# Kernel tuning notes

Measured on AMD Instinct MI355X. Metric: run time of the kernel, lower is better.

Reference implementation:

```python
import jax, jax.numpy as jnp
import numpy as np

CROP_H, CROP_W = 14, 14
MAX_BS = 64  # max boxes per image per level (MoldBatch padding)
NUM_LEVELS = 4


def _crop_and_resize(fmap, boxes, box_indices, ch, cw):
    """Bilinear tf.image.crop_and_resize equivalent.
    fmap: [B,H,W,C]; boxes: [N,4] normalized (y1,x1,y2,x2); box_indices: [N] int32.
    Returns [N,ch,cw,C]; samples outside the image get extrapolation value 0."""
    B, H, W, C = fmap.shape
    y1, x1, y2, x2 = boxes[:, 0], boxes[:, 1], boxes[:, 2], boxes[:, 3]
    ty = jnp.arange(ch, dtype=boxes.dtype) / (ch - 1)
    tx = jnp.arange(cw, dtype=boxes.dtype) / (cw - 1)
    ys = y1[:, None] * (H - 1) + ty[None, :] * ((y2 - y1)[:, None] * (H - 1))  # [N,ch]
    xs = x1[:, None] * (W - 1) + tx[None, :] * ((x2 - x1)[:, None] * (W - 1))  # [N,cw]
    y0f = jnp.floor(ys); x0f = jnp.floor(xs)
    wy = (ys - y0f)[:, :, None, None]  # [N,ch,1,1]
    wx = (xs - x0f)[:, None, :, None]  # [N,1,cw,1]
    y0 = jnp.clip(y0f.astype(jnp.int32), 0, H - 1); y1i = jnp.clip(y0 + 1, 0, H - 1)
    x0 = jnp.clip(x0f.astype(jnp.int32), 0, W - 1); x1i = jnp.clip(x0 + 1, 0, W - 1)
    bi = box_indices[:, None, None]
    g = lambda yi, xi: fmap[bi, yi[:, :, None], xi[:, None, :], :]  # [N,ch,cw,C]
    top = g(y0, x0) * (1 - wx) + g(y0, x1i) * wx
    bot = g(y1i, x0) * (1 - wx) + g(y1i, x1i) * wx
    out = top * (1 - wy) + bot * wy
    valid = ((ys >= 0) & (ys <= H - 1))[:, :, None] & ((xs >= 0) & (xs <= W - 1))[:, None, :]
    return out * valid[..., None].astype(out.dtype)


def setup_inputs() -> dict:
    key = jax.random.key(0)
    ks = jax.random.split(key, 8)
    B, N, C = 4, 128, 256
    sizes = [256, 128, 64, 32]
    inp = {}
    for i, s in enumerate(sizes):
        inp[f"fmap{i}"] = jax.random.normal(ks[i], (B, s, s, C), dtype=jnp.float32)
    ids = jax.random.randint(ks[4], (B, N), 0, NUM_LEVELS).astype(jnp.float32)
    cxy = jax.random.uniform(ks[5], (B, N, 2), minval=0.0, maxval=1024.0)
    wh = jax.random.uniform(ks[6], (B, N, 2), minval=16.0, maxval=256.0)
    cls_id = jnp.zeros((B, N, 1), jnp.float32)
    conf = jnp.full((B, N, 1), 0.9, jnp.float32)
    inp["dist_boxes"] = jnp.concatenate([ids[..., None], cxy, wh, cls_id, conf], axis=-1)
    inp["images"] = jnp.zeros((B, 1024, 1024, 3), jnp.float32)
    return inp


def _forward(fmaps, dist_boxes, images):
    B, N, _ = dist_boxes.shape
    Hi, Wi = images.shape[1], images.shape[2]
    cx, cy, w, h = (dist_boxes[..., 1], dist_boxes[..., 2], dist_boxes[..., 3], dist_boxes[..., 4])
    # NormalizeBoxes: (cx,cy,w,h) pixels -> normalized (y1,x1,y2,x2) for crop_and_resize
    norm_boxes = jnp.stack([
        (cy - h / 2) / (Hi - 1), (cx - w / 2) / (Wi - 1),
        (cy + h / 2) / (Hi - 1), (cx + w / 2) / (Wi - 1)], axis=-1)  # [B,N,4]
    ids = dist_boxes[..., 0]
    flat_boxes = norm_boxes.reshape(B * N, 4)
    box_idx = jnp.repeat(jnp.arange(B, dtype=jnp.int32), N)
    b_idx = jnp.broadcast_to(jnp.arange(B)[:, None], (B, N))
    boxes6 = dist_boxes[..., 1:]  # [B,N,6]
    roi_fmaps, roi_boxes = [], []
    for lvl, fmap in enumerate(fmaps):
        C = fmap.shape[-1]
        mask = ids == lvl  # [B,N] level routing (tf.where/gather_nd equivalent)
        crops = _crop_and_resize(fmap, flat_boxes, box_idx, CROP_H, CROP_W)
        crops = crops.reshape(B, N, CROP_H, CROP_W, C)
        # MoldBatch: scatter level-l boxes densely per image, zero-padded to MAX_BS
        rank = jnp.cumsum(mask.astype(jnp.int32), axis=1) - 1
        dest = jnp.where(mask & (rank < MAX_BS), rank, MAX_BS)  # overflow -> dump slot
        pf = jnp.zeros((B, MAX_BS + 1, CROP_H, CROP_W, C), crops.dtype)
        pf = pf.at[b_idx, dest].set(crops * mask[..., None, None, None].astype(crops.dtype))
        roi_fmaps.append(pf[:, :MAX_BS])
        pb = jnp.zeros((B, MAX_BS + 1, 6), dist_boxes.dtype)
        pb = pb.at[b_idx, dest].set(boxes6 * mask[..., None].astype(boxes6.dtype))
        roi_boxes.append(pb[:, :MAX_BS])
    return jnp.stack(roi_fmaps), jnp.concatenate(roi_boxes, axis=1)


def reference(fmap0, fmap1, fmap2, fmap3, dist_boxes, images):
    return _forward([fmap0, fmap1, fmap2, fmap3], dist_boxes, images)
```

## Files before the change

### kernel.cpp

```cpp
#include <hip/hip_runtime.h>

#define CROP 14
#define MAXBS 64
#define NLVL 4
#define BDIM 4
#define NBOX 128
#define CCH 256

__global__ void roi_meta_kernel(const float* __restrict__ db,
                                int* __restrict__ slot_map,
                                float* __restrict__ out1) {
    int b = blockIdx.x;
    int t = threadIdx.x;
    __shared__ int lvl_arr[NBOX];
    __shared__ int smap[NLVL * MAXBS];

    if (t < NBOX) {
        lvl_arr[t] = (int)db[(b * NBOX + t) * 7 + 0];
    }
    smap[t] = -1;
    __syncthreads();

    if (t < NLVL) {
        int r = 0;
        for (int n = 0; n < NBOX; ++n) {
            if (lvl_arr[n] == t) {
                if (r < MAXBS) smap[t * MAXBS + r] = n;
                r++;
            }
        }
    }
    __syncthreads();

    int n = smap[t];
    int lvl = t >> 6;
    int slot = t & 63;
    slot_map[(lvl * BDIM + b) * MAXBS + slot] = n;

    float* o = out1 + ((size_t)(b * (NLVL * MAXBS) + t)) * 6;
    if (n >= 0) {
        const float* src = db + (b * NBOX + n) * 7 + 1;
        #pragma unroll
        for (int j = 0; j < 6; ++j) o[j] = src[j];
    } else {
        #pragma unroll
        for (int j = 0; j < 6; ++j) o[j] = 0.f;
    }
}

__global__ void roi_crop_kernel(const float* __restrict__ f0,
                                const float* __restrict__ f1,
                                const float* __restrict__ f2,
                                const float* __restrict__ f3,
                                const float* __restrict__ db,
                                const int* __restrict__ slot_map,
                                float* __restrict__ out0) {
    int bid = blockIdx.x;
    int y  = bid % CROP;
    int sl = bid / CROP;
    int c  = threadIdx.x;

    float* out = out0 + ((size_t)(sl * CROP + y)) * CROP * CCH;

    int n = slot_map[sl];
    if (n < 0) {
        #pragma unroll
        for (int x = 0; x < CROP; ++x) out[x * CCH + c] = 0.f;
        return;
    }

    int lvl = sl >> 8;
    int b   = (sl >> 6) & 3;
    int s   = 256 >> lvl;
    const float* f = (lvl == 0) ? f0 : (lvl == 1) ? f1 : (lvl == 2) ? f2 : f3;

    const float* bx = db + (b * NBOX + n) * 7;
    float cx = bx[1], cy = bx[2], w = bx[3], h = bx[4];

    float y1n = (cy - h * 0.5f) / 1023.0f;
    float x1n = (cx - w * 0.5f) / 1023.0f;
    float y2n = (cy + h * 0.5f) / 1023.0f;
    float x2n = (cx + w * 0.5f) / 1023.0f;

    float Hm1 = (float)(s - 1);
    float ty = (float)y / 13.0f;
    float ys = y1n * Hm1 + ty * ((y2n - y1n) * Hm1);
    float y0f = floorf(ys);
    float wy = ys - y0f;
    int iy0 = (int)y0f;
    iy0 = iy0 < 0 ? 0 : (iy0 > s - 1 ? s - 1 : iy0);
    int iy1 = iy0 + 1;
    if (iy1 > s - 1) iy1 = s - 1;
    bool vy = (ys >= 0.f) && (ys <= Hm1);

    const float* rowT = f + ((size_t)(b * s + iy0)) * s * CCH;
    const float* rowB = f + ((size_t)(b * s + iy1)) * s * CCH;

    float x1nH   = x1n * Hm1;
    float xscale = (x2n - x1n) * Hm1;
    float omwy = 1.f - wy;

    #pragma unroll
    for (int x = 0; x < CROP; ++x) {
        float xs = x1nH + ((float)x / 13.0f) * xscale;
        float x0f = floorf(xs);
        float wx = xs - x0f;
        int ix0 = (int)x0f;
        ix0 = ix0 < 0 ? 0 : (ix0 > s - 1 ? s - 1 : ix0);
        int ix1 = ix0 + 1;
        if (ix1 > s - 1) ix1 = s - 1;
        bool vx = (xs >= 0.f) && (xs <= Hm1);

        float a  = rowT[ix0 * CCH + c];
        float bv = rowT[ix1 * CCH + c];
        float cv = rowB[ix0 * CCH + c];
        float dv = rowB[ix1 * CCH + c];

        float omwx = 1.f - wx;
        float top = a  * omwx + bv * wx;
        float bot = cv * omwx + dv * wx;
        float v   = top * omwy + bot * wy;

        out[x * CCH + c] = (vy && vx) ? v : 0.f;
    }
}

extern "C" void kernel_launch(void* const* d_in, const int* in_sizes, int n_in,
                              void* d_out, int out_size, void* d_ws, size_t ws_size,
                              hipStream_t stream) {
    const float* f0 = (const float*)d_in[0];
    const float* f1 = (const float*)d_in[1];
    const float* f2 = (const float*)d_in[2];
    const float* f3 = (const float*)d_in[3];
    const float* db = (const float*)d_in[4];

    float* out0 = (float*)d_out;
    float* out1 = out0 + (size_t)NLVL * BDIM * MAXBS * CROP * CROP * CCH;
    int* slot_map = (int*)d_ws;

    roi_meta_kernel<<<BDIM, 256, 0, stream>>>(db, slot_map, out1);
    roi_crop_kernel<<<NLVL * BDIM * MAXBS * CROP, 256, 0, stream>>>(
        f0, f1, f2, f3, db, slot_map, out0);
}
```

Before: 464.5 us.

## Vectorize crop kernel to float4 channels and remap blocks across XCDs

Each thread now handles four channels with 128-bit loads and stores, and the four wavefronts of a block split the 14 x-samples between them instead of looping over all of them. Block IDs are also remapped so that consecutive logical blocks (same crop row and box) land on the same XCD, which should improve L2 locality for the shared feature rows. The aim is fewer memory instructions and better cache reuse on a kernel that is bound by writing and gathering memory. The cost is uneven work per wave (14 x-samples over 4 groups) and a block schedule that depends on the grid dividing evenly by 8.

```diff
diff --git a/kernel.cpp b/kernel.cpp
--- a/kernel.cpp
+++ b/kernel.cpp
@@ -6,6 +6,12 @@
 #define BDIM 4
 #define NBOX 128
 #define CCH 256
+#define NSL (NLVL * BDIM * MAXBS)
+#define NBLK (NSL * CROP)
+#define NXCD 8
+#define CPX (NBLK / NXCD)
+
+typedef float f32x4 __attribute__((ext_vector_type(4)));
 
 __global__ void roi_meta_kernel(const float* __restrict__ db,
                                 int* __restrict__ slot_map,
@@ -48,24 +54,29 @@
     }
 }
 
-__global__ void roi_crop_kernel(const float* __restrict__ f0,
-                                const float* __restrict__ f1,
-                                const float* __restrict__ f2,
-                                const float* __restrict__ f3,
-                                const float* __restrict__ db,
-                                const int* __restrict__ slot_map,
-                                float* __restrict__ out0) {
-    int bid = blockIdx.x;
-    int y  = bid % CROP;
-    int sl = bid / CROP;
-    int c  = threadIdx.x;
+__global__ __launch_bounds__(256) void roi_crop_kernel(
+        const float* __restrict__ f0,
+        const float* __restrict__ f1,
+        const float* __restrict__ f2,
+        const float* __restrict__ f3,
+        const float* __restrict__ db,
+        const int* __restrict__ slot_map,
+        float* __restrict__ out0) {
+    int orig = blockIdx.x;
+    int wid  = (orig & (NXCD - 1)) * CPX + (orig >> 3);
+    int y  = wid % CROP;
+    int sl = wid / CROP;
+    int t  = threadIdx.x;
+    int cq = t & 63;
+    int xg = t >> 6;
 
-    float* out = out0 + ((size_t)(sl * CROP + y)) * CROP * CCH;
+    f32x4* out = (f32x4*)(out0 + ((size_t)(sl * CROP + y)) * CROP * CCH);
 
     int n = slot_map[sl];
     if (n < 0) {
+        f32x4 z = {0.f, 0.f, 0.f, 0.f};
         #pragma unroll
-        for (int x = 0; x < CROP; ++x) out[x * CCH + c] = 0.f;
+        for (int x = xg; x < CROP; x += 4) out[x * 64 + cq] = z;
         return;
     }
 
@@ -93,15 +104,15 @@
     if (iy1 > s - 1) iy1 = s - 1;
     bool vy = (ys >= 0.f) && (ys <= Hm1);
 
-    const float* rowT = f + ((size_t)(b * s + iy0)) * s * CCH;
-    const float* rowB = f + ((size_t)(b * s + iy1)) * s * CCH;
+    const f32x4* rowT = (const f32x4*)(f + ((size_t)(b * s + iy0)) * s * CCH);
+    const f32x4* rowB = (const f32x4*)(f + ((size_t)(b * s + iy1)) * s * CCH);
 
     float x1nH   = x1n * Hm1;
     float xscale = (x2n - x1n) * Hm1;
     float omwy = 1.f - wy;
 
     #pragma unroll
-    for (int x = 0; x < CROP; ++x) {
+    for (int x = xg; x < CROP; x += 4) {
         float xs = x1nH + ((float)x / 13.0f) * xscale;
         float x0f = floorf(xs);
         float wx = xs - x0f;
@@ -111,17 +122,18 @@
         if (ix1 > s - 1) ix1 = s - 1;
         bool vx = (xs >= 0.f) && (xs <= Hm1);
 
-        float a  = rowT[ix0 * CCH + c];
-        float bv = rowT[ix1 * CCH + c];
-        float cv = rowB[ix0 * CCH + c];
-        float dv = rowB[ix1 * CCH + c];
+        f32x4 a  = rowT[ix0 * 64 + cq];
+        f32x4 bv = rowT[ix1 * 64 + cq];
+        f32x4 cv = rowB[ix0 * 64 + cq];
+        f32x4 dv = rowB[ix1 * 64 + cq];
 
         float omwx = 1.f - wx;
-        float top = a  * omwx + bv * wx;
-        float bot = cv * omwx + dv * wx;
-        float v   = top * omwy + bot * wy;
+        f32x4 top = a  * omwx + bv * wx;
+        f32x4 bot = cv * omwx + dv * wx;
+        f32x4 v   = top * omwy + bot * wy;
 
-        out[x * CCH + c] = (vy && vx) ? v : 0.f;
+        if (!(vy && vx)) v = (f32x4){0.f, 0.f, 0.f, 0.f};
+        out[x * 64 + cq] = v;
     }
 }
 
@@ -135,10 +147,10 @@
     const float* db = (const float*)d_in[4];
 
     float* out0 = (float*)d_out;
-    float* out1 = out0 + (size_t)NLVL * BDIM * MAXBS * CROP * CROP * CCH;
+    float* out1 = out0 + (size_t)NSL * CROP * CROP * CCH;
     int* slot_map = (int*)d_ws;
 
     roi_meta_kernel<<<BDIM, 256, 0, stream>>>(db, slot_map, out1);
-    roi_crop_kernel<<<NLVL * BDIM * MAXBS * CROP, 256, 0, stream>>>(
+    roi_crop_kernel<<<NBLK, 256, 0, stream>>>(
         f0, f1, f2, f3, db, slot_map, out0);
 }
```

Result: slower. 476.5 us (+2.6%).
